# Performance work log

Measured on AMD Instinct MI355X. Metric: run time of the kernel, lower is better.

## Reference

```python
import jax, jax.numpy as jnp
import numpy as np

DIM = 2048
H = 16
KV_RANK = 512
NOPE = 128
ROPE_D = 64
VD = 128
QK = NOPE + ROPE_D  # 192
SCALE = QK ** -0.5
B, S = 2, 2048
EPS = 1e-5


def _rope(x, start_pos):
    # x: (b, s, h, d) or (b, s, d); rotate along last dim, positions along axis 1
    s = x.shape[1]
    d = x.shape[-1]
    half = d // 2
    inv_freq = 1.0 / (10000.0 ** (jnp.arange(half, dtype=jnp.float32) * (2.0 / d)))
    pos = jnp.arange(start_pos, start_pos + s, dtype=jnp.float32)
    ang = pos[:, None] * inv_freq[None, :]  # (s, half)
    cos, sin = jnp.cos(ang), jnp.sin(ang)
    if x.ndim == 4:
        cos, sin = cos[None, :, None, :], sin[None, :, None, :]
    else:
        cos, sin = cos[None, :, :], sin[None, :, :]
    x1, x2 = x[..., :half], x[..., half:]
    return jnp.concatenate([x1 * cos - x2 * sin, x2 * cos + x1 * sin], axis=-1).astype(x.dtype)


def _layernorm(x, w, b):
    mu = jnp.mean(x, axis=-1, keepdims=True)
    var = jnp.mean(jnp.square(x - mu), axis=-1, keepdims=True)
    return (x - mu) * jax.lax.rsqrt(var + EPS) * w + b


def setup_inputs() -> dict:
    key = jax.random.key(0)
    ks = jax.random.split(key, 6)
    std = 0.02
    x = jax.random.normal(ks[0], (B, S, DIM), dtype=jnp.float32)
    wq = jax.random.normal(ks[1], (H * QK, DIM), dtype=jnp.float32) * std
    wkv_a = jax.random.normal(ks[2], (KV_RANK + ROPE_D, DIM), dtype=jnp.float32) * std
    wkv_b = jax.random.normal(ks[3], (H * (NOPE + VD), KV_RANK), dtype=jnp.float32) * std
    wo = jax.random.normal(ks[4], (DIM, H * VD), dtype=jnp.float32) * std
    kv_norm_w = jnp.ones((KV_RANK,), dtype=jnp.float32)
    kv_norm_b = jnp.zeros((KV_RANK,), dtype=jnp.float32)
    return {"x": x, "wq": wq, "wkv_a": wkv_a, "kv_norm_w": kv_norm_w,
            "kv_norm_b": kv_norm_b, "wkv_b": wkv_b, "wo": wo, "start_pos": 0}


def reference(x, wq, wkv_a, kv_norm_w, kv_norm_b, wkv_b, wo, start_pos):
    b, s, _ = x.shape
    # query projection: (b,s,H,QK)
    q = (x @ wq.T).reshape(b, s, H, QK)
    q_nope, q_pe = q[..., :NOPE], q[..., NOPE:]
    q_pe = _rope(q_pe, start_pos)
    # compressed kv + rope key
    kv_all = x @ wkv_a.T                      # (b,s,KV_RANK+ROPE_D)
    kv, k_pe = kv_all[..., :KV_RANK], kv_all[..., KV_RANK:]
    k_pe = _rope(k_pe, start_pos)             # (b,s,ROPE_D)
    kvn = _layernorm(kv, kv_norm_w, kv_norm_b)  # (b,s,KV_RANK)
    # absorb path: expand compressed kv through per-head wkv_b blocks
    w = wkv_b.reshape(H, NOPE + VD, KV_RANK)
    k_nope = jnp.einsum('btc,hdc->bthd', kvn, w[:, :NOPE])   # (b,t,H,NOPE)
    v = jnp.einsum('btc,hdc->bthd', kvn, w[:, NOPE:])        # (b,t,H,VD)
    q_full = jnp.concatenate([q_nope, q_pe], axis=-1)        # (b,s,H,QK)
    k_full = jnp.concatenate(
        [k_nope, jnp.broadcast_to(k_pe[:, :, None, :], (b, s, H, ROPE_D))], axis=-1)
    scores = jnp.einsum('bshd,bthd->bhst', q_full, k_full) * SCALE
    causal = jnp.tril(jnp.ones((s, s), dtype=bool))
    scores = jnp.where(causal[None, None], scores, jnp.float32(-1e30))
    attn = jax.nn.softmax(scores, axis=-1)
    out = jnp.einsum('bhst,bthd->bshd', attn, v).reshape(b, s, H * VD)
    return out @ wo.T
```

## Files before the change

### kernel.cpp

```cpp
#include <hip/hip_runtime.h>
#include <hip/hip_bf16.h>
#include <math.h>

typedef __bf16 bf16_t;
typedef __bf16 bf16x2 __attribute__((ext_vector_type(2)));
typedef __bf16 bf16x4 __attribute__((ext_vector_type(4)));
typedef __bf16 bf16x8 __attribute__((ext_vector_type(8)));
typedef float f32x4 __attribute__((ext_vector_type(4)));

#define SEQ 2048
#define MLA_SCALE 0.07216878364870322f
#define LN_EPS 1e-5f

__device__ __forceinline__ void gload_lds16(const bf16_t* g, bf16_t* l) {
    __builtin_amdgcn_global_load_lds(
        (const __attribute__((address_space(1))) uint32_t*)(const void*)g,
        (__attribute__((address_space(3))) uint32_t*)(void*)l, 16, 0, 0);
}

__device__ __forceinline__ void xcd_map(int bid, int total, int nbn,
                                        int& bm, int& bn) {
    int per = total >> 3;
    int cbm = per / nbn;
    int xcd = bid & 7, s = bid >> 3;
    int q = s / nbn;
    bm = xcd * cbm + q;
    bn = s - q * nbn;
}

#define CVT_N0 2097152
#define CVT_N1 1572864
#define CVT_N2 294912
#define CVT_N3 524288
#define CVT_N4 1048576
#define CVT_TOT (CVT_N0 + CVT_N1 + CVT_N2 + CVT_N3 + CVT_N4)

__global__ __launch_bounds__(256)
void cvt_all(const float* __restrict__ x, const float* __restrict__ wq,
             const float* __restrict__ wa, const float* __restrict__ wb,
             const float* __restrict__ wo, bf16_t* __restrict__ xb,
             bf16_t* __restrict__ wqb, bf16_t* __restrict__ wab,
             bf16_t* __restrict__ wbb, bf16_t* __restrict__ wob) {
    for (int i = blockIdx.x * 256 + threadIdx.x; i < CVT_TOT; i += gridDim.x * 256) {
        const float* src; bf16_t* dst; int off = i;
        if (i < CVT_N0) { src = x; dst = xb; }
        else if (i < CVT_N0 + CVT_N1) { src = wq; dst = wqb; off = i - CVT_N0; }
        else if (i < CVT_N0 + CVT_N1 + CVT_N2) { src = wa; dst = wab; off = i - CVT_N0 - CVT_N1; }
        else if (i < CVT_N0 + CVT_N1 + CVT_N2 + CVT_N3) { src = wb; dst = wbb; off = i - CVT_N0 - CVT_N1 - CVT_N2; }
        else { src = wo; dst = wob; off = i - CVT_N0 - CVT_N1 - CVT_N2 - CVT_N3; }
        float4 v = ((const float4*)src)[off];
        bf16x4 p = { (bf16_t)v.x, (bf16_t)v.y, (bf16_t)v.z, (bf16_t)v.w };
        ((bf16x4*)dst)[off] = p;
    }
}

#define G256_PHASE(TAU, KS, MH, HTO, MAT, WAITV)                               \
{                                                                              \
    const int slot_ = (2 * (TAU) + (KS)) & 3;                                  \
    bf16x8 af_[4];                                                             \
    {                                                                          \
        const bf16_t* ab_ = As + slot_ * 8192 +                                \
                            (wm2 * 128 + (MH) * 64 + lr) * 32 + rdcol;         \
        _Pragma("unroll")                                                      \
        for (int f = 0; f < 4; ++f) af_[f] = *(const bf16x8*)(ab_ + f * 512);  \
    }                                                                          \
    if ((MH) == 0) {                                                           \
        const bf16_t* bb_ = Bs + slot_ * 8192 + (wn2 * 64 + lr) * 32 + rdcol;  \
        _Pragma("unroll")                                                      \
        for (int f = 0; f < 4; ++f) bq[f] = *(const bf16x8*)(bb_ + f * 512);   \
    }                                                                          \
    if ((MAT) == 0) stageA(2 * T + 3 + (HTO)); else stageB(2 * T + 3 + (HTO)); \
    __builtin_amdgcn_s_barrier();                                              \
    asm volatile("" ::: "memory");                                             \
    __builtin_amdgcn_s_setprio(1);                                             \
    _Pragma("unroll")                                                          \
    for (int f = 0; f < 4; ++f)                                                \
        _Pragma("unroll")                                                      \
        for (int n = 0; n < 4; ++n)                                            \
            acc[(MH) * 4 + f][n] = __builtin_amdgcn_mfma_f32_16x16x32_bf16(    \
                af_[f], bq[n], acc[(MH) * 4 + f][n], 0, 0, 0);                 \
    __builtin_amdgcn_s_setprio(0);                                             \
    asm volatile("" ::: "memory");                                             \
    if (WAITV) asm volatile("s_waitcnt vmcnt(8)" ::: "memory");                \
    __builtin_amdgcn_s_barrier();                                              \
}

template<int MODE>
__global__ __launch_bounds__(512, 2)
void gemm256(const bf16_t* __restrict__ A, const bf16_t* __restrict__ B,
             float* __restrict__ C, bf16_t* __restrict__ out0,
             bf16_t* __restrict__ out1, int N, int K, int total, int nbn) {
    __shared__ __attribute__((aligned(16))) bf16_t As[32768];
    __shared__ __attribute__((aligned(16))) bf16_t Bs[32768];
    __shared__ __attribute__((aligned(16))) bf16_t Ds[8192];

    const int tid = threadIdx.x;
    const int lane = tid & 63, w = tid >> 6;
    const int lr = lane & 15, kh = lane >> 4;
    const int wm2 = w >> 2, wn2 = w & 3;
    int bm, bn;
    xcd_map(blockIdx.x, total, nbn, bm, bn);
    const int NT = K >> 6;

    const int rdcol = 8 * (kh ^ ((lr >> 1) & 3));
    const int strow = (w << 5) + (lane >> 2);
    const int scol = 8 * ((lane & 3) ^ ((lane >> 3) & 3));

    f32x4 acc[8][4];
    #pragma unroll
    for (int i = 0; i < 8; ++i)
        #pragma unroll
        for (int j = 0; j < 4; ++j) acc[i][j] = 0.0f;

    auto stageA = [&](int ht) {
        int hs = (ht < 2 * NT) ? ht : (2 * NT - 1);
        int tau = hs >> 1, kap = hs & 1;
        const bf16_t* g = A + (size_t)(bm * 256 + strow) * K + tau * 64 + kap * 32 + scol;
        bf16_t* l = (ht < 2 * NT) ? (As + (ht & 3) * 8192 + w * 1024) : (Ds + w * 1024);
        gload_lds16(g, l);
        gload_lds16(g + (size_t)16 * K, l + 512);
    };
    auto stageB = [&](int ht) {
        int hs = (ht < 2 * NT) ? ht : (2 * NT - 1);
        int tau = hs >> 1, kap = hs & 1;
        const bf16_t* g = B + (size_t)(bn * 256 + strow) * K + tau * 64 + kap * 32 + scol;
        bf16_t* l = (ht < 2 * NT) ? (Bs + (ht & 3) * 8192 + w * 1024) : (Ds + w * 1024);
        gload_lds16(g, l);
        gload_lds16(g + (size_t)16 * K, l + 512);
    };

    stageA(0); stageB(0); stageA(1); stageB(1); stageA(2); stageB(2);
    asm volatile("s_waitcnt vmcnt(8)" ::: "memory");
    __builtin_amdgcn_s_barrier();

    for (int it = 0; it < (NT >> 1); ++it) {
        const int T = 2 * it;
        bf16x8 bq[4];
        G256_PHASE(T,     0, 0, 0, 0, 0)
        G256_PHASE(T,     0, 1, 0, 1, 1)
        G256_PHASE(T,     1, 0, 1, 0, 0)
        G256_PHASE(T,     1, 1, 1, 1, 1)
        G256_PHASE(T + 1, 0, 0, 2, 0, 0)
        G256_PHASE(T + 1, 0, 1, 2, 1, 1)
        G256_PHASE(T + 1, 1, 0, 3, 0, 0)
        G256_PHASE(T + 1, 1, 1, 3, 1, 1)
    }

    const int rg = kh * 4;
    if (MODE == 0) {
        #pragma unroll
        for (int mf = 0; mf < 8; ++mf)
            #pragma unroll
            for (int nf = 0; nf < 4; ++nf) {
                size_t row0 = (size_t)(bm * 256 + wm2 * 128 + mf * 16 + rg);
                int col = bn * 256 + wn2 * 64 + nf * 16 + lr;
                #pragma unroll
                for (int rr = 0; rr < 4; ++rr)
                    C[(row0 + rr) * N + col] = acc[mf][nf][rr];
            }
    } else if (MODE == 1) {
        const int h = bn;
        #pragma unroll
        for (int mf = 0; mf < 8; ++mf)
            #pragma unroll
            for (int nf = 0; nf < 4; ++nf) {
                int d = wn2 * 64 + nf * 16 + lr;
                int trow = bm * 256 + wm2 * 128 + mf * 16 + rg;
                int b = trow >> 11, t = trow & 2047;
                if (d < 128) {
                    bf16_t* p = out0 + ((size_t)(b * 16 + h) * SEQ + t) * 192 + d;
                    #pragma unroll
                    for (int rr = 0; rr < 4; ++rr)
                        p[rr * 192] = (bf16_t)acc[mf][nf][rr];
                } else {
                    bf16x4 pv = { (bf16_t)acc[mf][nf][0], (bf16_t)acc[mf][nf][1],
                                  (bf16_t)acc[mf][nf][2], (bf16_t)acc[mf][nf][3] };
                    *(bf16x4*)(out1 + ((size_t)(b * 16 + h) * 128 + (d - 128)) * SEQ + t) = pv;
                }
            }
    } else {
        #pragma unroll
        for (int mf = 0; mf < 8; ++mf)
            #pragma unroll
            for (int nf = 0; nf < 4; ++nf) {
                int n = bn * 256 + wn2 * 64 + nf * 16 + lr;
                int h = n / 192, d = n - h * 192;
                int trow = bm * 256 + wm2 * 128 + mf * 16 + rg;
                int b = trow >> 11, t = trow & 2047;
                bf16_t* p = out0 + ((size_t)(b * 16 + h) * SEQ + t) * 192 + d;
                #pragma unroll
                for (int rr = 0; rr < 4; ++rr)
                    p[rr * 192] = (bf16_t)acc[mf][nf][rr];
            }
    }
}

__global__ __launch_bounds__(256)
void gemm_nt(const bf16_t* __restrict__ A, const bf16_t* __restrict__ B,
             float* __restrict__ C, int M, int N, int K, int total, int nbn) {
    __shared__ bf16_t As[4096], Bs[4096];
    int bm, bn;
    xcd_map(blockIdx.x, total, nbn, bm, bn);

    const int tid = threadIdx.x;
    const int lane = tid & 63, w = tid >> 6;
    const int lr = lane & 15, kh = lane >> 4;
    const int wm = (w >> 1) * 64, wn = (w & 1) * 64;
    const int subrow = lane >> 2;
    const int colel = (lane & 3) * 8;

    f32x4 acc[4][4];
    #pragma unroll
    for (int i = 0; i < 4; ++i)
        #pragma unroll
        for (int j = 0; j < 4; ++j) acc[i][j] = 0.0f;

    const int rA = bm * 128 + 32 * w + subrow;
    const int rB = bn * 128 + 32 * w + subrow;
    const int rb1 = (rB < N) ? rB : (N - 1);
    const int rb2 = (rB + 16 < N) ? (rB + 16) : (N - 1);

    for (int kt = 0; kt < K; kt += 32) {
        __syncthreads();
        gload_lds16(A + (size_t)rA * K + kt + colel,        As + (2 * w) * 512);
        gload_lds16(A + (size_t)(rA + 16) * K + kt + colel, As + (2 * w + 1) * 512);
        gload_lds16(B + (size_t)rb1 * K + kt + colel,       Bs + (2 * w) * 512);
        gload_lds16(B + (size_t)rb2 * K + kt + colel,       Bs + (2 * w + 1) * 512);
        __syncthreads();
        bf16x8 af[4], bfr[4];
        #pragma unroll
        for (int im = 0; im < 4; ++im)
            af[im] = *(const bf16x8*)(As + (wm + im * 16 + lr) * 32 + kh * 8);
        #pragma unroll
        for (int jn = 0; jn < 4; ++jn)
            bfr[jn] = *(const bf16x8*)(Bs + (wn + jn * 16 + lr) * 32 + kh * 8);
        #pragma unroll
        for (int im = 0; im < 4; ++im)
            #pragma unroll
            for (int jn = 0; jn < 4; ++jn)
                acc[im][jn] = __builtin_amdgcn_mfma_f32_16x16x32_bf16(
                    af[im], bfr[jn], acc[im][jn], 0, 0, 0);
    }

    const int rg = kh * 4;
    #pragma unroll
    for (int im = 0; im < 4; ++im)
        #pragma unroll
        for (int jn = 0; jn < 4; ++jn) {
            int col = bn * 128 + wn + jn * 16 + lr;
            if (col >= N) continue;
            size_t rowb = (size_t)(bm * 128 + wm + im * 16 + rg);
            #pragma unroll
            for (int rr = 0; rr < 4; ++rr)
                C[(rowb + rr) * N + col] = acc[im][jn][rr];
        }
}

__global__ __launch_bounds__(256)
void rope_ln(const float* __restrict__ kv_all,
             const float* __restrict__ lnw, const float* __restrict__ lnb,
             bf16_t* __restrict__ kvnb, bf16_t* __restrict__ kpack,
             float2* __restrict__ rope_cs, const int* __restrict__ start_pos) {
    const int m = blockIdx.x;
    const int tid = threadIdx.x;
    const int b = m >> 11, t = m & 2047;
    const float pos = (float)(start_pos[0] + t);
    __shared__ float red[8];
    __shared__ float stats[2];
    __shared__ float kbuf[64];

    const float* kvrow = kv_all + (size_t)m * 576;
    float v0 = kvrow[tid], v1 = kvrow[tid + 256];
    float ssum = v0 + v1, ssq = v0 * v0 + v1 * v1;
    for (int off = 32; off > 0; off >>= 1) {
        ssum += __shfl_down(ssum, off);
        ssq  += __shfl_down(ssq, off);
    }
    const int lane = tid & 63, wid = tid >> 6;
    if (lane == 0) { red[wid] = ssum; red[4 + wid] = ssq; }
    __syncthreads();
    if (tid == 0) {
        float ts = red[0] + red[1] + red[2] + red[3];
        float tq = red[4] + red[5] + red[6] + red[7];
        float mu = ts * (1.0f / 512.0f);
        float var = tq * (1.0f / 512.0f) - mu * mu;
        stats[0] = mu;
        stats[1] = rsqrtf(var + LN_EPS);
    }
    if (tid < 32) {
        int j = tid;
        float inv = expf(-(float)j * 0.2878231366242554f);
        float ang = pos * inv;
        float c = cosf(ang), sn = sinf(ang);
        float x1 = kvrow[512 + j], x2 = kvrow[544 + j];
        kbuf[j]      = x1 * c - x2 * sn;
        kbuf[32 + j] = x2 * c + x1 * sn;
        if (b == 0) rope_cs[t * 32 + j] = make_float2(c, sn);
    }
    __syncthreads();
    float mu = stats[0], rstd = stats[1];
    kvnb[(size_t)m * 512 + tid]       = (bf16_t)((v0 - mu) * rstd * lnw[tid] + lnb[tid]);
    kvnb[(size_t)m * 512 + tid + 256] = (bf16_t)((v1 - mu) * rstd * lnw[tid + 256] + lnb[tid + 256]);

    {
        int hh = tid >> 4, j4 = (tid & 15) * 4;
        bf16x4 pk = { (bf16_t)kbuf[j4], (bf16_t)kbuf[j4 + 1],
                      (bf16_t)kbuf[j4 + 2], (bf16_t)kbuf[j4 + 3] };
        *(bf16x4*)(kpack + ((size_t)(b * 16 + hh) * SEQ + t) * 192 + 128 + j4) = pk;
    }
}

__global__ __launch_bounds__(256, 3)
void attn_mfma(const bf16_t* __restrict__ qb, const bf16_t* __restrict__ kpack,
               const bf16_t* __restrict__ vt, const float2* __restrict__ rope_cs,
               bf16_t* __restrict__ ao) {
    __shared__ bf16_t Ks[64 * 192];
    __shared__ bf16_t Vts[128 * 64];
    __shared__ bf16_t Pls[4 * 16 * 64];

    const int bid = blockIdx.x;
    const int xcd = bid & 7, s = bid >> 3;
    const int g = xcd * 4 + (s >> 5);
    const int qt = 31 - (s & 31);
    const int h = g & 15, b = g >> 4;

    const int tid = threadIdx.x;
    const int lane = tid & 63, w = tid >> 6;
    const int lr = lane & 15, kh = lane >> 4;
    const int lr7 = lr & 7;
    const int e0 = kh ^ lr7;
    const int e1 = (4 + kh) ^ lr7;
    const size_t bS = (size_t)b * SEQ;
    const bf16_t* kbase = kpack + (size_t)(b * 16 + h) * SEQ * 192;
    const bf16_t* vbase = vt + (size_t)(b * 16 + h) * 128 * SEQ;

    int kgo_[6], klo_[6], vgo_[4], vlo_[4];
    #pragma unroll
    for (int i = 0; i < 6; ++i) {
        int c = tid + 256 * i;
        int row = c / 24, slot = c % 24;
        kgo_[i] = row * 192 + slot * 8;
        klo_[i] = row * 192 + ((slot & 24) | ((slot ^ row) & 7)) * 8;
    }
    #pragma unroll
    for (int i = 0; i < 4; ++i) {
        int c = tid + 256 * i;
        int row = c >> 3, slot = c & 7;
        vgo_[i] = row;
        vlo_[i] = row * 64 + (slot ^ (row & 7)) * 8;
    }
    int vco_[4];
    #pragma unroll
    for (int i = 0; i < 4; ++i) vco_[i] = (tid + 256 * i) & 7;

    const int q0 = qt * 64;
    const int myrow = q0 + w * 16;
    const int qabs = myrow + lr;

    bf16x8 qf[6];
    {
        const bf16_t* qrow = qb + ((size_t)(b * 16 + h) * SEQ + qabs) * 192;
        #pragma unroll
        for (int ks = 0; ks < 6; ++ks)
            qf[ks] = *(const bf16x8*)(qrow + ks * 32 + kh * 8);
        const float2* csp = rope_cs + (size_t)qabs * 32 + kh * 8;
        #pragma unroll
        for (int i = 0; i < 8; ++i) {
            float2 cs = csp[i];
            float x1 = (float)qf[4][i], x2 = (float)qf[5][i];
            qf[4][i] = (bf16_t)(x1 * cs.x - x2 * cs.y);
            qf[5][i] = (bf16_t)(x2 * cs.x + x1 * cs.y);
        }
    }

    f32x4 O[8];
    #pragma unroll
    for (int i = 0; i < 8; ++i) O[i] = 0.0f;
    float m_r = -1e30f, l_r = 0.0f;

    bf16x8 rk[6], rv[4];
    #pragma unroll
    for (int i = 0; i < 6; ++i)
        rk[i] = *(const bf16x8*)(kbase + kgo_[i]);
    #pragma unroll
    for (int i = 0; i < 4; ++i)
        rv[i] = *(const bf16x8*)(vbase + (size_t)vgo_[i] * SEQ + vco_[i] * 8);

    for (int kt = 0; kt <= qt; ++kt) {
        __syncthreads();
        #pragma unroll
        for (int i = 0; i < 6; ++i) *(bf16x8*)(Ks + klo_[i]) = rk[i];
        #pragma unroll
        for (int i = 0; i < 4; ++i) *(bf16x8*)(Vts + vlo_[i]) = rv[i];
        if (kt < qt) {
            const int t1 = (kt + 1) * 64;
            #pragma unroll
            for (int i = 0; i < 6; ++i)
                rk[i] = *(const bf16x8*)(kbase + (size_t)t1 * 192 + kgo_[i]);
            #pragma unroll
            for (int i = 0; i < 4; ++i)
                rv[i] = *(const bf16x8*)(vbase + (size_t)vgo_[i] * SEQ + t1 + vco_[i] * 8);
        }
        __syncthreads();

        f32x4 sacc[4];
        #pragma unroll
        for (int j = 0; j < 4; ++j) sacc[j] = 0.0f;
        __builtin_amdgcn_s_setprio(1);
        #pragma unroll
        for (int ks = 0; ks < 6; ++ks) {
            const int sw = (ks >> 1) * 64 + ((ks & 1) ? e1 : e0) * 8;
            #pragma unroll
            for (int j = 0; j < 4; ++j) {
                bf16x8 kf = *(const bf16x8*)(Ks + (j * 16 + lr) * 192 + sw);
                sacc[j] = __builtin_amdgcn_mfma_f32_16x16x32_bf16(kf, qf[ks], sacc[j], 0, 0, 0);
            }
        }
        __builtin_amdgcn_s_setprio(0);

        const int t0 = kt * 64;
        float p[16];
        if (kt == qt) {
            #pragma unroll
            for (int j = 0; j < 4; ++j)
                #pragma unroll
                for (int rr = 0; rr < 4; ++rr) {
                    int tabs = t0 + j * 16 + kh * 4 + rr;
                    p[j * 4 + rr] = (tabs > qabs) ? -1e30f : sacc[j][rr] * MLA_SCALE;
                }
        } else {
            #pragma unroll
            for (int j = 0; j < 4; ++j)
                #pragma unroll
                for (int rr = 0; rr < 4; ++rr)
                    p[j * 4 + rr] = sacc[j][rr] * MLA_SCALE;
        }

        float mx = p[0];
        #pragma unroll
        for (int e = 1; e < 16; ++e) mx = fmaxf(mx, p[e]);
        mx = fmaxf(mx, __shfl_xor(mx, 16));
        mx = fmaxf(mx, __shfl_xor(mx, 32));

        if (!__all(mx <= m_r + 8.0f)) {
            float mnew = fmaxf(m_r, mx);
            float cr = __expf(m_r - mnew);
            l_r *= cr;
            m_r = mnew;
            float corr[4];
            #pragma unroll
            for (int rr = 0; rr < 4; ++rr)
                corr[rr] = __shfl(cr, kh * 4 + rr);
            #pragma unroll
            for (int dt = 0; dt < 8; ++dt)
                #pragma unroll
                for (int rr = 0; rr < 4; ++rr)
                    O[dt][rr] *= corr[rr];
        }

        float ps = 0.0f;
        #pragma unroll
        for (int e = 0; e < 16; ++e) {
            p[e] = __expf(p[e] - m_r);
            ps += p[e];
        }
        ps += __shfl_xor(ps, 16);
        ps += __shfl_xor(ps, 32);
        l_r += ps;

        bf16_t* pw = Pls + (w * 16 + lr) * 64;
        const int f2 = kh >> 1, h4 = (kh & 1) * 4;
        #pragma unroll
        for (int j = 0; j < 4; ++j) {
            bf16x4 pp = { (bf16_t)p[j * 4], (bf16_t)p[j * 4 + 1],
                          (bf16_t)p[j * 4 + 2], (bf16_t)p[j * 4 + 3] };
            *(bf16x4*)(pw + ((2 * j + f2) ^ lr7) * 8 + h4) = pp;
        }
        bf16x8 pa0 = *(const bf16x8*)(pw + e0 * 8);
        bf16x8 pa1 = *(const bf16x8*)(pw + e1 * 8);
        __builtin_amdgcn_s_setprio(1);
        #pragma unroll
        for (int dt = 0; dt < 8; ++dt) {
            bf16x8 b0 = *(const bf16x8*)(Vts + (dt * 16 + lr) * 64 + e0 * 8);
            O[dt] = __builtin_amdgcn_mfma_f32_16x16x32_bf16(pa0, b0, O[dt], 0, 0, 0);
            bf16x8 b1 = *(const bf16x8*)(Vts + (dt * 16 + lr) * 64 + e1 * 8);
            O[dt] = __builtin_amdgcn_mfma_f32_16x16x32_bf16(pa1, b1, O[dt], 0, 0, 0);
        }
        __builtin_amdgcn_s_setprio(0);
    }

    float linv[4];
    #pragma unroll
    for (int rr = 0; rr < 4; ++rr)
        linv[rr] = 1.0f / __shfl(l_r, kh * 4 + rr);
    #pragma unroll
    for (int rr = 0; rr < 4; ++rr) {
        size_t rowb = (bS + myrow + kh * 4 + rr) * 2048 + h * 128;
        #pragma unroll
        for (int dt = 0; dt < 8; ++dt)
            ao[rowb + dt * 16 + lr] = (bf16_t)(O[dt][rr] * linv[rr]);
    }
}

extern "C" void kernel_launch(void* const* d_in, const int* in_sizes, int n_in,
                              void* d_out, int out_size, void* d_ws, size_t ws_size,
                              hipStream_t stream) {
    const float* x     = (const float*)d_in[0];
    const float* wq    = (const float*)d_in[1];
    const float* wkv_a = (const float*)d_in[2];
    const float* lnw   = (const float*)d_in[3];
    const float* lnb   = (const float*)d_in[4];
    const float* wkv_b = (const float*)d_in[5];
    const float* wo    = (const float*)d_in[6];
    const int* start_pos = (const int*)d_in[7];
    float* out = (float*)d_out;

    char* w8 = (char*)d_ws;
    bf16_t* xb   = (bf16_t*)(w8);
    bf16_t* wqb  = (bf16_t*)(w8 + 16777216);
    bf16_t* wab  = (bf16_t*)(w8 + 29360128);
    bf16_t* wbb  = (bf16_t*)(w8 + 31719424);
    bf16_t* wob  = (bf16_t*)(w8 + 35913728);
    bf16_t* kvnb = (bf16_t*)(w8 + 44302336);
    bf16_t* kpk  = (bf16_t*)(w8 + 48496640);
    bf16_t* vtb  = (bf16_t*)(w8 + 73662464);
    bf16_t* aob  = (bf16_t*)(w8 + 90439680);
    bf16_t* qbh  = (bf16_t*)(w8 + 107216896);
    float*  kva  = (float*)(w8 + 132382720);
    float2* rcs  = (float2*)(w8 + 141819904);

    cvt_all<<<2048, 256, 0, stream>>>(x, wq, wkv_a, wkv_b, wo, xb, wqb, wab, wbb, wob);

    gemm256<2><<<192, 512, 0, stream>>>(xb, wqb, nullptr, qbh, nullptr, 3072, 2048, 192, 12);
    gemm_nt<<<160, 256, 0, stream>>>(xb, wab, kva, 4096, 576, 2048, 160, 5);
    rope_ln<<<4096, 256, 0, stream>>>(kva, lnw, lnb, kvnb, kpk, rcs, start_pos);
    gemm256<1><<<256, 512, 0, stream>>>(kvnb, wbb, nullptr, kpk, vtb, 4096, 512, 256, 16);
    attn_mfma<<<1024, 256, 0, stream>>>(qbh, kpk, vtb, rcs, aob);
    gemm_nt<<<512, 256, 0, stream>>>(aob, wob, out, 4096, 2048, 2048, 512, 16);
}
```

Baseline: 301.2 us.

## Pair causal query tiles per block and double-buffer K tiles in attention

Each attention block now handles two query tiles, qt and 31-qt, so every block gets the same amount of causal work, and the grid is halved to 512 blocks. K tiles are double-buffered in shared memory with a two-tile-ahead register prefetch. V staging is moved to after the softmax, which splits the barriers differently. The aim is to remove causal tail imbalance and hide load latency. In exchange, occupancy drops to 2 blocks per CU, shared memory use grows, and register pressure rises.

```diff
diff --git a/kernel.cpp b/kernel.cpp
--- a/kernel.cpp
+++ b/kernel.cpp
@@ -310,18 +310,18 @@
     }
 }
 
-__global__ __launch_bounds__(256, 3)
+__global__ __launch_bounds__(256, 2)
 void attn_mfma(const bf16_t* __restrict__ qb, const bf16_t* __restrict__ kpack,
                const bf16_t* __restrict__ vt, const float2* __restrict__ rope_cs,
                bf16_t* __restrict__ ao) {
-    __shared__ bf16_t Ks[64 * 192];
+    __shared__ bf16_t Ks[2][64 * 192];
     __shared__ bf16_t Vts[128 * 64];
     __shared__ bf16_t Pls[4 * 16 * 64];
 
     const int bid = blockIdx.x;
     const int xcd = bid & 7, s = bid >> 3;
-    const int g = xcd * 4 + (s >> 5);
-    const int qt = 31 - (s & 31);
+    const int g = xcd * 4 + (s >> 4);
+    const int bx = s & 15;
     const int h = g & 15, b = g >> 4;
 
     const int tid = threadIdx.x;
@@ -334,7 +334,7 @@
     const bf16_t* kbase = kpack + (size_t)(b * 16 + h) * SEQ * 192;
     const bf16_t* vbase = vt + (size_t)(b * 16 + h) * 128 * SEQ;
 
-    int kgo_[6], klo_[6], vgo_[4], vlo_[4];
+    int kgo_[6], klo_[6], vgo_[4], vlo_[4], vco_[4];
     #pragma unroll
     for (int i = 0; i < 6; ++i) {
         int c = tid + 256 * i;
@@ -348,157 +348,184 @@
         int row = c >> 3, slot = c & 7;
         vgo_[i] = row;
         vlo_[i] = row * 64 + (slot ^ (row & 7)) * 8;
-    }
-    int vco_[4];
-    #pragma unroll
-    for (int i = 0; i < 4; ++i) vco_[i] = (tid + 256 * i) & 7;
-
-    const int q0 = qt * 64;
-    const int myrow = q0 + w * 16;
-    const int qabs = myrow + lr;
-
-    bf16x8 qf[6];
-    {
-        const bf16_t* qrow = qb + ((size_t)(b * 16 + h) * SEQ + qabs) * 192;
-        #pragma unroll
-        for (int ks = 0; ks < 6; ++ks)
-            qf[ks] = *(const bf16x8*)(qrow + ks * 32 + kh * 8);
-        const float2* csp = rope_cs + (size_t)qabs * 32 + kh * 8;
-        #pragma unroll
-        for (int i = 0; i < 8; ++i) {
-            float2 cs = csp[i];
-            float x1 = (float)qf[4][i], x2 = (float)qf[5][i];
-            qf[4][i] = (bf16_t)(x1 * cs.x - x2 * cs.y);
-            qf[5][i] = (bf16_t)(x2 * cs.x + x1 * cs.y);
+        vco_[i] = slot;
+    }
+
+    for (int half = 0; half < 2; ++half) {
+        const int qt = half ? bx : (31 - bx);
+        const int q0 = qt * 64;
+        const int myrow = q0 + w * 16;
+        const int qabs = myrow + lr;
+
+        bf16x8 qf[6];
+        {
+            const bf16_t* qrow = qb + ((size_t)(b * 16 + h) * SEQ + qabs) * 192;
+            #pragma unroll
+            for (int ks = 0; ks < 6; ++ks)
+                qf[ks] = *(const bf16x8*)(qrow + ks * 32 + kh * 8);
+            const float2* csp = rope_cs + (size_t)qabs * 32 + kh * 8;
+            #pragma unroll
+            for (int i = 0; i < 8; ++i) {
+                float2 cs = csp[i];
+                float x1 = (float)qf[4][i], x2 = (float)qf[5][i];
+                qf[4][i] = (bf16_t)(x1 * cs.x - x2 * cs.y);
+                qf[5][i] = (bf16_t)(x2 * cs.x + x1 * cs.y);
+            }
         }
-    }
-
-    f32x4 O[8];
-    #pragma unroll
-    for (int i = 0; i < 8; ++i) O[i] = 0.0f;
-    float m_r = -1e30f, l_r = 0.0f;
-
-    bf16x8 rk[6], rv[4];
-    #pragma unroll
-    for (int i = 0; i < 6; ++i)
-        rk[i] = *(const bf16x8*)(kbase + kgo_[i]);
-    #pragma unroll
-    for (int i = 0; i < 4; ++i)
-        rv[i] = *(const bf16x8*)(vbase + (size_t)vgo_[i] * SEQ + vco_[i] * 8);
-
-    for (int kt = 0; kt <= qt; ++kt) {
-        __syncthreads();
-        #pragma unroll
-        for (int i = 0; i < 6; ++i) *(bf16x8*)(Ks + klo_[i]) = rk[i];
-        #pragma unroll
-        for (int i = 0; i < 4; ++i) *(bf16x8*)(Vts + vlo_[i]) = rv[i];
-        if (kt < qt) {
-            const int t1 = (kt + 1) * 64;
+
+        f32x4 O[8];
+        #pragma unroll
+        for (int i = 0; i < 8; ++i) O[i] = 0.0f;
+        float m_r = -1e30f, l_r = 0.0f;
+
+        bf16x8 rkw[6], rkl[6], rv[4];
+        {
+            bf16x8 rk0[6];
             #pragma unroll
             for (int i = 0; i < 6; ++i)
-                rk[i] = *(const bf16x8*)(kbase + (size_t)t1 * 192 + kgo_[i]);
+                rk0[i] = *(const bf16x8*)(kbase + kgo_[i]);
+            #pragma unroll
+            for (int i = 0; i < 6; ++i)
+                *(bf16x8*)(Ks[0] + klo_[i]) = rk0[i];
+        }
+        {
+            const int t1 = (qt > 0 ? 1 : 0) * 64;
+            #pragma unroll
+            for (int i = 0; i < 6; ++i)
+                rkw[i] = *(const bf16x8*)(kbase + (size_t)t1 * 192 + kgo_[i]);
             #pragma unroll
             for (int i = 0; i < 4; ++i)
-                rv[i] = *(const bf16x8*)(vbase + (size_t)vgo_[i] * SEQ + t1 + vco_[i] * 8);
+                rv[i] = *(const bf16x8*)(vbase + (size_t)vgo_[i] * SEQ + vco_[i] * 8);
         }
         __syncthreads();
 
-        f32x4 sacc[4];
-        #pragma unroll
-        for (int j = 0; j < 4; ++j) sacc[j] = 0.0f;
-        __builtin_amdgcn_s_setprio(1);
-        #pragma unroll
-        for (int ks = 0; ks < 6; ++ks) {
-            const int sw = (ks >> 1) * 64 + ((ks & 1) ? e1 : e0) * 8;
+        for (int kt = 0; kt <= qt; ++kt) {
+            const int cur = kt & 1;
+            const bf16_t* ksc = Ks[cur];
+            bf16_t* ksn = Ks[cur ^ 1];
+
+            if (kt < qt) {
+                #pragma unroll
+                for (int i = 0; i < 6; ++i)
+                    *(bf16x8*)(ksn + klo_[i]) = rkw[i];
+            }
+            {
+                const int tl = (kt + 2 <= qt ? kt + 2 : qt) * 64;
+                #pragma unroll
+                for (int i = 0; i < 6; ++i)
+                    rkl[i] = *(const bf16x8*)(kbase + (size_t)tl * 192 + kgo_[i]);
+            }
+
+            f32x4 sacc[4];
+            #pragma unroll
+            for (int j = 0; j < 4; ++j) sacc[j] = 0.0f;
+            __builtin_amdgcn_s_setprio(1);
+            #pragma unroll
+            for (int ks = 0; ks < 6; ++ks) {
+                const int sw = (ks >> 1) * 64 + ((ks & 1) ? e1 : e0) * 8;
+                #pragma unroll
+                for (int j = 0; j < 4; ++j) {
+                    bf16x8 kf = *(const bf16x8*)(ksc + (j * 16 + lr) * 192 + sw);
+                    sacc[j] = __builtin_amdgcn_mfma_f32_16x16x32_bf16(kf, qf[ks], sacc[j], 0, 0, 0);
+                }
+            }
+            __builtin_amdgcn_s_setprio(0);
+
+            const int t0 = kt * 64;
+            float p[16];
+            if (kt == qt) {
+                #pragma unroll
+                for (int j = 0; j < 4; ++j)
+                    #pragma unroll
+                    for (int rr = 0; rr < 4; ++rr) {
+                        int tabs = t0 + j * 16 + kh * 4 + rr;
+                        p[j * 4 + rr] = (tabs > qabs) ? -1e30f : sacc[j][rr] * MLA_SCALE;
+                    }
+            } else {
+                #pragma unroll
+                for (int j = 0; j < 4; ++j)
+                    #pragma unroll
+                    for (int rr = 0; rr < 4; ++rr)
+                        p[j * 4 + rr] = sacc[j][rr] * MLA_SCALE;
+            }
+
+            float mx = p[0];
+            #pragma unroll
+            for (int e = 1; e < 16; ++e) mx = fmaxf(mx, p[e]);
+            mx = fmaxf(mx, __shfl_xor(mx, 16));
+            mx = fmaxf(mx, __shfl_xor(mx, 32));
+
+            if (!__all(mx <= m_r + 8.0f)) {
+                float mnew = fmaxf(m_r, mx);
+                float cr = __expf(m_r - mnew);
+                l_r *= cr;
+                m_r = mnew;
+                float corr[4];
+                #pragma unroll
+                for (int rr = 0; rr < 4; ++rr)
+                    corr[rr] = __shfl(cr, kh * 4 + rr);
+                #pragma unroll
+                for (int dt = 0; dt < 8; ++dt)
+                    #pragma unroll
+                    for (int rr = 0; rr < 4; ++rr)
+                        O[dt][rr] *= corr[rr];
+            }
+
+            float ps = 0.0f;
+            #pragma unroll
+            for (int e = 0; e < 16; ++e) {
+                p[e] = __expf(p[e] - m_r);
+                ps += p[e];
+            }
+            ps += __shfl_xor(ps, 16);
+            ps += __shfl_xor(ps, 32);
+            l_r += ps;
+
+            __syncthreads();
+            #pragma unroll
+            for (int i = 0; i < 4; ++i) *(bf16x8*)(Vts + vlo_[i]) = rv[i];
+            {
+                const int tv = (kt + 1 <= qt ? kt + 1 : qt) * 64;
+                #pragma unroll
+                for (int i = 0; i < 4; ++i)
+                    rv[i] = *(const bf16x8*)(vbase + (size_t)vgo_[i] * SEQ + tv + vco_[i] * 8);
+            }
+            bf16_t* pw = Pls + (w * 16 + lr) * 64;
+            const int f2 = kh >> 1, h4 = (kh & 1) * 4;
             #pragma unroll
             for (int j = 0; j < 4; ++j) {
-                bf16x8 kf = *(const bf16x8*)(Ks + (j * 16 + lr) * 192 + sw);
-                sacc[j] = __builtin_amdgcn_mfma_f32_16x16x32_bf16(kf, qf[ks], sacc[j], 0, 0, 0);
-            }
+                bf16x4 pp = { (bf16_t)p[j * 4], (bf16_t)p[j * 4 + 1],
+                              (bf16_t)p[j * 4 + 2], (bf16_t)p[j * 4 + 3] };
+                *(bf16x4*)(pw + ((2 * j + f2) ^ lr7) * 8 + h4) = pp;
+            }
+            __syncthreads();
+            bf16x8 pa0 = *(const bf16x8*)(pw + e0 * 8);
+            bf16x8 pa1 = *(const bf16x8*)(pw + e1 * 8);
+            __builtin_amdgcn_s_setprio(1);
+            #pragma unroll
+            for (int dt = 0; dt < 8; ++dt) {
+                bf16x8 b0 = *(const bf16x8*)(Vts + (dt * 16 + lr) * 64 + e0 * 8);
+                O[dt] = __builtin_amdgcn_mfma_f32_16x16x32_bf16(pa0, b0, O[dt], 0, 0, 0);
+                bf16x8 b1 = *(const bf16x8*)(Vts + (dt * 16 + lr) * 64 + e1 * 8);
+                O[dt] = __builtin_amdgcn_mfma_f32_16x16x32_bf16(pa1, b1, O[dt], 0, 0, 0);
+            }
+            __builtin_amdgcn_s_setprio(0);
+            #pragma unroll
+            for (int i = 0; i < 6; ++i) rkw[i] = rkl[i];
         }
-        __builtin_amdgcn_s_setprio(0);
-
-        const int t0 = kt * 64;
-        float p[16];
-        if (kt == qt) {
-            #pragma unroll
-            for (int j = 0; j < 4; ++j)
-                #pragma unroll
-                for (int rr = 0; rr < 4; ++rr) {
-                    int tabs = t0 + j * 16 + kh * 4 + rr;
-                    p[j * 4 + rr] = (tabs > qabs) ? -1e30f : sacc[j][rr] * MLA_SCALE;
-                }
-        } else {
-            #pragma unroll
-            for (int j = 0; j < 4; ++j)
-                #pragma unroll
-                for (int rr = 0; rr < 4; ++rr)
-                    p[j * 4 + rr] = sacc[j][rr] * MLA_SCALE;
+
+        float linv[4];
+        #pragma unroll
+        for (int rr = 0; rr < 4; ++rr)
+            linv[rr] = 1.0f / __shfl(l_r, kh * 4 + rr);
+        #pragma unroll
+        for (int rr = 0; rr < 4; ++rr) {
+            size_t rowb = (bS + myrow + kh * 4 + rr) * 2048 + h * 128;
+            #pragma unroll
+            for (int dt = 0; dt < 8; ++dt)
+                ao[rowb + dt * 16 + lr] = (bf16_t)(O[dt][rr] * linv[rr]);
         }
-
-        float mx = p[0];
-        #pragma unroll
-        for (int e = 1; e < 16; ++e) mx = fmaxf(mx, p[e]);
-        mx = fmaxf(mx, __shfl_xor(mx, 16));
-        mx = fmaxf(mx, __shfl_xor(mx, 32));
-
-        if (!__all(mx <= m_r + 8.0f)) {
-            float mnew = fmaxf(m_r, mx);
-            float cr = __expf(m_r - mnew);
-            l_r *= cr;
-            m_r = mnew;
-            float corr[4];
-            #pragma unroll
-            for (int rr = 0; rr < 4; ++rr)
-                corr[rr] = __shfl(cr, kh * 4 + rr);
-            #pragma unroll
-            for (int dt = 0; dt < 8; ++dt)
-                #pragma unroll
-                for (int rr = 0; rr < 4; ++rr)
-                    O[dt][rr] *= corr[rr];
-        }
-
-        float ps = 0.0f;
-        #pragma unroll
-        for (int e = 0; e < 16; ++e) {
-            p[e] = __expf(p[e] - m_r);
-            ps += p[e];
-        }
-        ps += __shfl_xor(ps, 16);
-        ps += __shfl_xor(ps, 32);
-        l_r += ps;
-
-        bf16_t* pw = Pls + (w * 16 + lr) * 64;
-        const int f2 = kh >> 1, h4 = (kh & 1) * 4;
-        #pragma unroll
-        for (int j = 0; j < 4; ++j) {
-            bf16x4 pp = { (bf16_t)p[j * 4], (bf16_t)p[j * 4 + 1],
-                          (bf16_t)p[j * 4 + 2], (bf16_t)p[j * 4 + 3] };
-            *(bf16x4*)(pw + ((2 * j + f2) ^ lr7) * 8 + h4) = pp;
-        }
-        bf16x8 pa0 = *(const bf16x8*)(pw + e0 * 8);
-        bf16x8 pa1 = *(const bf16x8*)(pw + e1 * 8);
-        __builtin_amdgcn_s_setprio(1);
-        #pragma unroll
-        for (int dt = 0; dt < 8; ++dt) {
-            bf16x8 b0 = *(const bf16x8*)(Vts + (dt * 16 + lr) * 64 + e0 * 8);
-            O[dt] = __builtin_amdgcn_mfma_f32_16x16x32_bf16(pa0, b0, O[dt], 0, 0, 0);
-            bf16x8 b1 = *(const bf16x8*)(Vts + (dt * 16 + lr) * 64 + e1 * 8);
-            O[dt] = __builtin_amdgcn_mfma_f32_16x16x32_bf16(pa1, b1, O[dt], 0, 0, 0);
-        }
-        __builtin_amdgcn_s_setprio(0);
-    }
-
-    float linv[4];
-    #pragma unroll
-    for (int rr = 0; rr < 4; ++rr)
-        linv[rr] = 1.0f / __shfl(l_r, kh * 4 + rr);
-    #pragma unroll
-    for (int rr = 0; rr < 4; ++rr) {
-        size_t rowb = (bS + myrow + kh * 4 + rr) * 2048 + h * 128;
-        #pragma unroll
-        for (int dt = 0; dt < 8; ++dt)
-            ao[rowb + dt * 16 + lr] = (bf16_t)(O[dt][rr] * linv[rr]);
+        __syncthreads();
     }
 }
 
@@ -535,6 +562,6 @@
     gemm_nt<<<160, 256, 0, stream>>>(xb, wab, kva, 4096, 576, 2048, 160, 5);
     rope_ln<<<4096, 256, 0, stream>>>(kva, lnw, lnb, kvnb, kpk, rcs, start_pos);
     gemm256<1><<<256, 512, 0, stream>>>(kvnb, wbb, nullptr, kpk, vtb, 4096, 512, 256, 16);
-    attn_mfma<<<1024, 256, 0, stream>>>(qbh, kpk, vtb, rcs, aob);
+    attn_mfma<<<512, 256, 0, stream>>>(qbh, kpk, vtb, rcs, aob);
     gemm_nt<<<512, 256, 0, stream>>>(aob, wob, out, 4096, 2048, 2048, 512, 16);
 }
```

Result: faster. 275.0 us (median of 3 runs) (-8.7%).

## Restructure attention: 2 waves x 32 rows, paired causal tiles, async LDS double-buffer

Applied to the files above, without the earlier changes.

Rewrites the attention kernel to use 128-thread blocks in which each wave handles 32 query rows (two 16-row groups sharing each K fragment). Each block processes two complementary causal query tiles (31-bx and bx) for load balance across 512 blocks. K/V tiles are now loaded with global_load_lds directly into LDS, with K double-buffered and prefetched during compute instead of staged through registers. This aims to raise K reuse per LDS read and overlap loads with MFMA work, at the cost of higher register pressure and fewer waves per block.

```diff
diff --git a/kernel.cpp b/kernel.cpp
--- a/kernel.cpp
+++ b/kernel.cpp
@@ -310,19 +310,19 @@
     }
 }
 
-__global__ __launch_bounds__(256, 3)
+__global__ __launch_bounds__(128)
 void attn_mfma(const bf16_t* __restrict__ qb, const bf16_t* __restrict__ kpack,
                const bf16_t* __restrict__ vt, const float2* __restrict__ rope_cs,
                bf16_t* __restrict__ ao) {
-    __shared__ bf16_t Ks[64 * 192];
-    __shared__ bf16_t Vts[128 * 64];
-    __shared__ bf16_t Pls[4 * 16 * 64];
+    __shared__ __attribute__((aligned(16))) bf16_t Ks[2][64 * 192];
+    __shared__ __attribute__((aligned(16))) bf16_t Vts[128 * 64];
+    __shared__ __attribute__((aligned(16))) bf16_t Pls[2 * 32 * 64];
 
     const int bid = blockIdx.x;
     const int xcd = bid & 7, s = bid >> 3;
-    const int g = xcd * 4 + (s >> 5);
-    const int qt = 31 - (s & 31);
-    const int h = g & 15, b = g >> 4;
+    const int grp = xcd * 4 + (s >> 4);
+    const int bx = s & 15;
+    const int h = grp & 15, b = grp >> 4;
 
     const int tid = threadIdx.x;
     const int lane = tid & 63, w = tid >> 6;
@@ -334,171 +334,194 @@
     const bf16_t* kbase = kpack + (size_t)(b * 16 + h) * SEQ * 192;
     const bf16_t* vbase = vt + (size_t)(b * 16 + h) * 128 * SEQ;
 
-    int kgo_[6], klo_[6], vgo_[4], vlo_[4];
+    int kgo_[12];
     #pragma unroll
-    for (int i = 0; i < 6; ++i) {
-        int c = tid + 256 * i;
-        int row = c / 24, slot = c % 24;
-        kgo_[i] = row * 192 + slot * 8;
-        klo_[i] = row * 192 + ((slot & 24) | ((slot ^ row) & 7)) * 8;
-    }
+    for (int i = 0; i < 12; ++i) {
+        int c = tid + 128 * i;
+        int row = c / 24, sl = c % 24;
+        kgo_[i] = row * 192 + ((sl & 24) | ((sl ^ row) & 7)) * 8;
+    }
+    int vgo_[8];
     #pragma unroll
-    for (int i = 0; i < 4; ++i) {
-        int c = tid + 256 * i;
-        int row = c >> 3, slot = c & 7;
-        vgo_[i] = row;
-        vlo_[i] = row * 64 + (slot ^ (row & 7)) * 8;
-    }
-    int vco_[4];
-    #pragma unroll
-    for (int i = 0; i < 4; ++i) vco_[i] = (tid + 256 * i) & 7;
-
-    const int q0 = qt * 64;
-    const int myrow = q0 + w * 16;
-    const int qabs = myrow + lr;
-
-    bf16x8 qf[6];
-    {
-        const bf16_t* qrow = qb + ((size_t)(b * 16 + h) * SEQ + qabs) * 192;
-        #pragma unroll
-        for (int ks = 0; ks < 6; ++ks)
-            qf[ks] = *(const bf16x8*)(qrow + ks * 32 + kh * 8);
-        const float2* csp = rope_cs + (size_t)qabs * 32 + kh * 8;
-        #pragma unroll
-        for (int i = 0; i < 8; ++i) {
-            float2 cs = csp[i];
-            float x1 = (float)qf[4][i], x2 = (float)qf[5][i];
-            qf[4][i] = (bf16_t)(x1 * cs.x - x2 * cs.y);
-            qf[5][i] = (bf16_t)(x2 * cs.x + x1 * cs.y);
+    for (int i = 0; i < 8; ++i) {
+        int c = tid + 128 * i;
+        int d = c >> 3, sl = c & 7;
+        vgo_[i] = d * SEQ + ((sl ^ (d & 7)) * 8);
+    }
+
+    for (int half = 0; half < 2; ++half) {
+        const int qt = half ? bx : (31 - bx);
+        const int q0 = qt * 64;
+        int qabs[2];
+        qabs[0] = q0 + w * 32 + lr;
+        qabs[1] = q0 + w * 32 + 16 + lr;
+
+        bf16x8 qf[2][6];
+        #pragma unroll
+        for (int g = 0; g < 2; ++g) {
+            const bf16_t* qrow = qb + ((size_t)(b * 16 + h) * SEQ + qabs[g]) * 192;
+            #pragma unroll
+            for (int ks = 0; ks < 6; ++ks)
+                qf[g][ks] = *(const bf16x8*)(qrow + ks * 32 + kh * 8);
+            const float2* csp = rope_cs + (size_t)qabs[g] * 32 + kh * 8;
+            #pragma unroll
+            for (int i = 0; i < 8; ++i) {
+                float2 cs = csp[i];
+                float x1 = (float)qf[g][4][i], x2 = (float)qf[g][5][i];
+                qf[g][4][i] = (bf16_t)(x1 * cs.x - x2 * cs.y);
+                qf[g][5][i] = (bf16_t)(x2 * cs.x + x1 * cs.y);
+            }
         }
-    }
-
-    f32x4 O[8];
-    #pragma unroll
-    for (int i = 0; i < 8; ++i) O[i] = 0.0f;
-    float m_r = -1e30f, l_r = 0.0f;
-
-    bf16x8 rk[6], rv[4];
-    #pragma unroll
-    for (int i = 0; i < 6; ++i)
-        rk[i] = *(const bf16x8*)(kbase + kgo_[i]);
-    #pragma unroll
-    for (int i = 0; i < 4; ++i)
-        rv[i] = *(const bf16x8*)(vbase + (size_t)vgo_[i] * SEQ + vco_[i] * 8);
-
-    for (int kt = 0; kt <= qt; ++kt) {
+
+        f32x4 O[2][8];
+        #pragma unroll
+        for (int g = 0; g < 2; ++g)
+            #pragma unroll
+            for (int i = 0; i < 8; ++i) O[g][i] = 0.0f;
+        float m_r[2] = { -1e30f, -1e30f }, l_r[2] = { 0.0f, 0.0f };
+
+        int cur = 0;
+        #pragma unroll
+        for (int i = 0; i < 12; ++i)
+            gload_lds16(kbase + kgo_[i], Ks[0] + (128 * i + 64 * w) * 8);
+        asm volatile("s_waitcnt vmcnt(0)" ::: "memory");
         __syncthreads();
-        #pragma unroll
-        for (int i = 0; i < 6; ++i) *(bf16x8*)(Ks + klo_[i]) = rk[i];
-        #pragma unroll
-        for (int i = 0; i < 4; ++i) *(bf16x8*)(Vts + vlo_[i]) = rv[i];
-        if (kt < qt) {
-            const int t1 = (kt + 1) * 64;
-            #pragma unroll
-            for (int i = 0; i < 6; ++i)
-                rk[i] = *(const bf16x8*)(kbase + (size_t)t1 * 192 + kgo_[i]);
-            #pragma unroll
-            for (int i = 0; i < 4; ++i)
-                rv[i] = *(const bf16x8*)(vbase + (size_t)vgo_[i] * SEQ + t1 + vco_[i] * 8);
+
+        for (int kt = 0; kt <= qt; ++kt) {
+            bf16_t* kcur = Ks[cur];
+            bf16_t* knxt = Ks[cur ^ 1];
+            #pragma unroll
+            for (int i = 0; i < 8; ++i)
+                gload_lds16(vbase + vgo_[i] + kt * 64, Vts + (128 * i + 64 * w) * 8);
+            const int tn = (kt + 1 <= qt) ? (kt + 1) : qt;
+            #pragma unroll
+            for (int i = 0; i < 12; ++i)
+                gload_lds16(kbase + (size_t)tn * 12288 + kgo_[i],
+                            knxt + (128 * i + 64 * w) * 8);
+
+            f32x4 sacc[2][4];
+            #pragma unroll
+            for (int g = 0; g < 2; ++g)
+                #pragma unroll
+                for (int j = 0; j < 4; ++j) sacc[g][j] = 0.0f;
+            __builtin_amdgcn_s_setprio(1);
+            #pragma unroll
+            for (int ks = 0; ks < 6; ++ks) {
+                const int sw = (ks >> 1) * 64 + ((ks & 1) ? e1 : e0) * 8;
+                #pragma unroll
+                for (int j = 0; j < 4; ++j) {
+                    bf16x8 kf = *(const bf16x8*)(kcur + (j * 16 + lr) * 192 + sw);
+                    sacc[0][j] = __builtin_amdgcn_mfma_f32_16x16x32_bf16(kf, qf[0][ks], sacc[0][j], 0, 0, 0);
+                    sacc[1][j] = __builtin_amdgcn_mfma_f32_16x16x32_bf16(kf, qf[1][ks], sacc[1][j], 0, 0, 0);
+                }
+            }
+            __builtin_amdgcn_s_setprio(0);
+
+            const int t0 = kt * 64;
+            const int f2 = kh >> 1, h4 = (kh & 1) * 4;
+            #pragma unroll
+            for (int g = 0; g < 2; ++g) {
+                float p[16];
+                if (kt == qt) {
+                    #pragma unroll
+                    for (int j = 0; j < 4; ++j)
+                        #pragma unroll
+                        for (int rr = 0; rr < 4; ++rr) {
+                            int tabs = t0 + j * 16 + kh * 4 + rr;
+                            p[j * 4 + rr] = (tabs > qabs[g]) ? -1e30f
+                                           : sacc[g][j][rr] * MLA_SCALE;
+                        }
+                } else {
+                    #pragma unroll
+                    for (int j = 0; j < 4; ++j)
+                        #pragma unroll
+                        for (int rr = 0; rr < 4; ++rr)
+                            p[j * 4 + rr] = sacc[g][j][rr] * MLA_SCALE;
+                }
+
+                float mx = p[0];
+                #pragma unroll
+                for (int e = 1; e < 16; ++e) mx = fmaxf(mx, p[e]);
+                mx = fmaxf(mx, __shfl_xor(mx, 16));
+                mx = fmaxf(mx, __shfl_xor(mx, 32));
+
+                if (!__all(mx <= m_r[g] + 8.0f)) {
+                    float mnew = fmaxf(m_r[g], mx);
+                    float cr = __expf(m_r[g] - mnew);
+                    l_r[g] *= cr;
+                    m_r[g] = mnew;
+                    float corr[4];
+                    #pragma unroll
+                    for (int rr = 0; rr < 4; ++rr)
+                        corr[rr] = __shfl(cr, kh * 4 + rr);
+                    #pragma unroll
+                    for (int dt = 0; dt < 8; ++dt)
+                        #pragma unroll
+                        for (int rr = 0; rr < 4; ++rr)
+                            O[g][dt][rr] *= corr[rr];
+                }
+
+                float ps = 0.0f;
+                #pragma unroll
+                for (int e = 0; e < 16; ++e) {
+                    p[e] = __expf(p[e] - m_r[g]);
+                    ps += p[e];
+                }
+                ps += __shfl_xor(ps, 16);
+                ps += __shfl_xor(ps, 32);
+                l_r[g] += ps;
+
+                bf16_t* pw = Pls + (w * 32 + g * 16 + lr) * 64;
+                #pragma unroll
+                for (int j = 0; j < 4; ++j) {
+                    bf16x4 pp = { (bf16_t)p[j * 4], (bf16_t)p[j * 4 + 1],
+                                  (bf16_t)p[j * 4 + 2], (bf16_t)p[j * 4 + 3] };
+                    *(bf16x4*)(pw + ((2 * j + f2) ^ lr7) * 8 + h4) = pp;
+                }
+            }
+
+            asm volatile("s_waitcnt vmcnt(12)" ::: "memory");
+            __syncthreads();
+
+            bf16x8 pa[2][2];
+            #pragma unroll
+            for (int g = 0; g < 2; ++g) {
+                const bf16_t* pw = Pls + (w * 32 + g * 16 + lr) * 64;
+                pa[g][0] = *(const bf16x8*)(pw + e0 * 8);
+                pa[g][1] = *(const bf16x8*)(pw + e1 * 8);
+            }
+            __builtin_amdgcn_s_setprio(1);
+            #pragma unroll
+            for (int dt = 0; dt < 8; ++dt) {
+                bf16x8 b0 = *(const bf16x8*)(Vts + (dt * 16 + lr) * 64 + e0 * 8);
+                bf16x8 b1 = *(const bf16x8*)(Vts + (dt * 16 + lr) * 64 + e1 * 8);
+                O[0][dt] = __builtin_amdgcn_mfma_f32_16x16x32_bf16(pa[0][0], b0, O[0][dt], 0, 0, 0);
+                O[0][dt] = __builtin_amdgcn_mfma_f32_16x16x32_bf16(pa[0][1], b1, O[0][dt], 0, 0, 0);
+                O[1][dt] = __builtin_amdgcn_mfma_f32_16x16x32_bf16(pa[1][0], b0, O[1][dt], 0, 0, 0);
+                O[1][dt] = __builtin_amdgcn_mfma_f32_16x16x32_bf16(pa[1][1], b1, O[1][dt], 0, 0, 0);
+            }
+            __builtin_amdgcn_s_setprio(0);
+
+            asm volatile("s_waitcnt vmcnt(0)" ::: "memory");
+            __syncthreads();
+            cur ^= 1;
+        }
+
+        #pragma unroll
+        for (int g = 0; g < 2; ++g) {
+            float linv[4];
+            #pragma unroll
+            for (int rr = 0; rr < 4; ++rr)
+                linv[rr] = 1.0f / __shfl(l_r[g], kh * 4 + rr);
+            #pragma unroll
+            for (int rr = 0; rr < 4; ++rr) {
+                size_t rowb = (bS + q0 + w * 32 + g * 16 + kh * 4 + rr) * 2048 + h * 128;
+                #pragma unroll
+                for (int dt = 0; dt < 8; ++dt)
+                    ao[rowb + dt * 16 + lr] = (bf16_t)(O[g][dt][rr] * linv[rr]);
+            }
         }
         __syncthreads();
-
-        f32x4 sacc[4];
-        #pragma unroll
-        for (int j = 0; j < 4; ++j) sacc[j] = 0.0f;
-        __builtin_amdgcn_s_setprio(1);
-        #pragma unroll
-        for (int ks = 0; ks < 6; ++ks) {
-            const int sw = (ks >> 1) * 64 + ((ks & 1) ? e1 : e0) * 8;
-            #pragma unroll
-            for (int j = 0; j < 4; ++j) {
-                bf16x8 kf = *(const bf16x8*)(Ks + (j * 16 + lr) * 192 + sw);
-                sacc[j] = __builtin_amdgcn_mfma_f32_16x16x32_bf16(kf, qf[ks], sacc[j], 0, 0, 0);
-            }
-        }
-        __builtin_amdgcn_s_setprio(0);
-
-        const int t0 = kt * 64;
-        float p[16];
-        if (kt == qt) {
-            #pragma unroll
-            for (int j = 0; j < 4; ++j)
-                #pragma unroll
-                for (int rr = 0; rr < 4; ++rr) {
-                    int tabs = t0 + j * 16 + kh * 4 + rr;
-                    p[j * 4 + rr] = (tabs > qabs) ? -1e30f : sacc[j][rr] * MLA_SCALE;
-                }
-        } else {
-            #pragma unroll
-            for (int j = 0; j < 4; ++j)
-                #pragma unroll
-                for (int rr = 0; rr < 4; ++rr)
-                    p[j * 4 + rr] = sacc[j][rr] * MLA_SCALE;
-        }
-
-        float mx = p[0];
-        #pragma unroll
-        for (int e = 1; e < 16; ++e) mx = fmaxf(mx, p[e]);
-        mx = fmaxf(mx, __shfl_xor(mx, 16));
-        mx = fmaxf(mx, __shfl_xor(mx, 32));
-
-        if (!__all(mx <= m_r + 8.0f)) {
-            float mnew = fmaxf(m_r, mx);
-            float cr = __expf(m_r - mnew);
-            l_r *= cr;
-            m_r = mnew;
-            float corr[4];
-            #pragma unroll
-            for (int rr = 0; rr < 4; ++rr)
-                corr[rr] = __shfl(cr, kh * 4 + rr);
-            #pragma unroll
-            for (int dt = 0; dt < 8; ++dt)
-                #pragma unroll
-                for (int rr = 0; rr < 4; ++rr)
-                    O[dt][rr] *= corr[rr];
-        }
-
-        float ps = 0.0f;
-        #pragma unroll
-        for (int e = 0; e < 16; ++e) {
-            p[e] = __expf(p[e] - m_r);
-            ps += p[e];
-        }
-        ps += __shfl_xor(ps, 16);
-        ps += __shfl_xor(ps, 32);
-        l_r += ps;
-
-        bf16_t* pw = Pls + (w * 16 + lr) * 64;
-        const int f2 = kh >> 1, h4 = (kh & 1) * 4;
-        #pragma unroll
-        for (int j = 0; j < 4; ++j) {
-            bf16x4 pp = { (bf16_t)p[j * 4], (bf16_t)p[j * 4 + 1],
-                          (bf16_t)p[j * 4 + 2], (bf16_t)p[j * 4 + 3] };
-            *(bf16x4*)(pw + ((2 * j + f2) ^ lr7) * 8 + h4) = pp;
-        }
-        bf16x8 pa0 = *(const bf16x8*)(pw + e0 * 8);
-        bf16x8 pa1 = *(const bf16x8*)(pw + e1 * 8);
-        __builtin_amdgcn_s_setprio(1);
-        #pragma unroll
-        for (int dt = 0; dt < 8; ++dt) {
-            bf16x8 b0 = *(const bf16x8*)(Vts + (dt * 16 + lr) * 64 + e0 * 8);
-            O[dt] = __builtin_amdgcn_mfma_f32_16x16x32_bf16(pa0, b0, O[dt], 0, 0, 0);
-            bf16x8 b1 = *(const bf16x8*)(Vts + (dt * 16 + lr) * 64 + e1 * 8);
-            O[dt] = __builtin_amdgcn_mfma_f32_16x16x32_bf16(pa1, b1, O[dt], 0, 0, 0);
-        }
-        __builtin_amdgcn_s_setprio(0);
-    }
-
-    float linv[4];
-    #pragma unroll
-    for (int rr = 0; rr < 4; ++rr)
-        linv[rr] = 1.0f / __shfl(l_r, kh * 4 + rr);
-    #pragma unroll
-    for (int rr = 0; rr < 4; ++rr) {
-        size_t rowb = (bS + myrow + kh * 4 + rr) * 2048 + h * 128;
-        #pragma unroll
-        for (int dt = 0; dt < 8; ++dt)
-            ao[rowb + dt * 16 + lr] = (bf16_t)(O[dt][rr] * linv[rr]);
     }
 }
 
@@ -535,6 +558,6 @@
     gemm_nt<<<160, 256, 0, stream>>>(xb, wab, kva, 4096, 576, 2048, 160, 5);
     rope_ln<<<4096, 256, 0, stream>>>(kva, lnw, lnb, kvnb, kpk, rcs, start_pos);
     gemm256<1><<<256, 512, 0, stream>>>(kvnb, wbb, nullptr, kpk, vtb, 4096, 512, 256, 16);
-    attn_mfma<<<1024, 256, 0, stream>>>(qbh, kpk, vtb, rcs, aob);
+    attn_mfma<<<512, 128, 0, stream>>>(qbh, kpk, vtb, rcs, aob);
     gemm_nt<<<512, 256, 0, stream>>>(aob, wob, out, 4096, 2048, 2048, 512, 16);
 }
```

Measured after the change: 305.4 us. No clear change (+1.4%).
